# Performance work log

Measured on AMD Instinct MI355X. Metric: run time of the kernel, lower is better.

Reference implementation:

```python
import jax, jax.numpy as jnp
import numpy as np

D_MODEL = 2048
NUM_HEADS = 16
HEAD_DIM = D_MODEL // NUM_HEADS  # 128
B, L = 2, 2048


def setup_inputs() -> dict:
    key = jax.random.key(0)
    ks = jax.random.split(key, 7)
    s = 0.02
    return {
        "x": jax.random.normal(ks[0], (B, L, D_MODEL), dtype=jnp.float32),
        "Wq_w": jax.random.normal(ks[1], (D_MODEL, D_MODEL), dtype=jnp.float32) * s,
        "Wq_b": jnp.zeros((D_MODEL,), dtype=jnp.float32),
        "Wk_w": jax.random.normal(ks[2], (HEAD_DIM, D_MODEL), dtype=jnp.float32) * s,
        "Wk_b": jnp.zeros((HEAD_DIM,), dtype=jnp.float32),
        "Wv_w": jax.random.normal(ks[3], (HEAD_DIM, D_MODEL), dtype=jnp.float32) * s,
        "Wv_b": jnp.zeros((HEAD_DIM,), dtype=jnp.float32),
    }


def reference(x, Wq_w, Wq_b, Wk_w, Wk_b, Wv_w, Wv_b):
    b, l, _ = x.shape
    # torch Linear: y = x @ W.T + b
    Q = (x @ Wq_w.T + Wq_b).reshape(b, l, NUM_HEADS, HEAD_DIM)  # [B,L,H,D]
    K = x @ Wk_w.T + Wk_b  # [B,L,D] single shared KV head (MQA)
    V = x @ Wv_w.T + Wv_b  # [B,L,D]
    scale = 1.0 / jnp.sqrt(jnp.float32(HEAD_DIM))
    # scores: [B,H,Lq,Lk]; K's head dim (size 1 in torch) broadcasts -> contract over d only
    scores = jnp.einsum("bqhd,bkd->bhqk", Q, K) * scale
    attn = jax.nn.softmax(scores, axis=-1)
    out = jnp.einsum("bhqk,bkd->bqhd", attn, V)  # [B,L,H,D]
    return out.reshape(b, l, D_MODEL)
```

## Files before the change

kernel.cpp:

```cpp
#include <hip/hip_runtime.h>
#include <hip/hip_bf16.h>


typedef unsigned short u16;
typedef unsigned int u32;
typedef __bf16 bf16x8 __attribute__((ext_vector_type(8)));
typedef float f32x16 __attribute__((ext_vector_type(16)));
typedef u16 u16x4 __attribute__((ext_vector_type(4)));
typedef u32 u32x4 __attribute__((ext_vector_type(4)));

#define MFMA32(a, b, c) __builtin_amdgcn_mfma_f32_32x32x16_bf16((a), (b), (c), 0, 0, 0)

__device__ __forceinline__ u16 f2bf(float f) {
  __hip_bfloat16 h = __float2bfloat16(f);
  return __builtin_bit_cast(u16, h);
}

__device__ __forceinline__ float fexp2(float x) {
#if __has_builtin(__builtin_amdgcn_exp2f)
  return __builtin_amdgcn_exp2f(x);
#else
  return exp2f(x);
#endif
}

__device__ __forceinline__ void cp16(const void* g, void* l) {
  __builtin_amdgcn_global_load_lds(
      (const __attribute__((address_space(1))) u32*)g,
      (__attribute__((address_space(3))) u32*)l, 16, 0, 0);
}

__device__ __forceinline__ f32x16 zero16() {
  f32x16 v;
#pragma unroll
  for (int i = 0; i < 16; ++i) v[i] = 0.f;
  return v;
}

__global__ __launch_bounds__(256) void k_convert(
    const float* __restrict__ x, const float* __restrict__ wq,
    const float* __restrict__ wk, const float* __restrict__ wv,
    u16* __restrict__ xb, u16* __restrict__ wqb,
    u16* __restrict__ wkb, u16* __restrict__ wvb) {
  int idx = blockIdx.x * 256 + threadIdx.x;
  for (int i = idx; i < 3276800; i += 524288) {
    float4 v; u16* dst;
    if (i < 2097152) {
      v = ((const float4*)x)[i]; dst = xb + (size_t)i * 4;
    } else if (i < 3145728) {
      int j = i - 2097152; v = ((const float4*)wq)[j]; dst = wqb + (size_t)j * 4;
    } else if (i < 3211264) {
      int j = i - 3145728; v = ((const float4*)wk)[j]; dst = wkb + (size_t)j * 4;
    } else {
      int j = i - 3211264; v = ((const float4*)wv)[j]; dst = wvb + (size_t)j * 4;
    }
    u16x4 o;
    o[0] = f2bf(v.x); o[1] = f2bf(v.y); o[2] = f2bf(v.z); o[3] = f2bf(v.w);
    *(u16x4*)dst = o;
  }
}

__global__ __launch_bounds__(256, 2) void k_gemm_qkv(
    const u16* __restrict__ xb, const u16* __restrict__ wqb,
    const u16* __restrict__ wkb, const u16* __restrict__ wvb,
    const float* __restrict__ bq, const float* __restrict__ bk, const float* __restrict__ bv,
    u16* __restrict__ qout, u16* __restrict__ kout, u16* __restrict__ vtout) {
  __shared__ __align__(16) u16 sh[36864];
  const int tid = threadIdx.x;
  const int w = tid >> 6, lane = tid & 63, ln = lane & 31, hi = lane >> 5;
  const int wr = w >> 1, wc = w & 1;
  const int m0 = blockIdx.x * 128;
  const int by = blockIdx.y;
  const int mode = (by < 16) ? 0 : (by - 15);
  const int n0loc = (mode == 0) ? by * 128 : 0;
  const u16* __restrict__ Bp = (mode == 0) ? wqb : (mode == 1 ? wkb : wvb);
  const u16* Arow = xb + (size_t)m0 * 2048;
  const u16* Brow = Bp + (size_t)n0loc * 2048;

  const u16* sb[9];
#pragma unroll
  for (int i = 0; i < 9; ++i) {
    int s = (w + i * 4) * 64 + lane;
    const u16* base; int r, c;
    if (s < 1152) { r = s / 9; c = s % 9; if (c > 7) c = 0; base = Arow; }
    else { int s2 = s - 1152; r = s2 / 9; c = s2 % 9; if (c > 7) c = 0; base = Brow; }
    sb[i] = base + (size_t)r * 2048 + c * 8;
  }

  f32x16 acc[2][2];
  acc[0][0] = zero16(); acc[0][1] = zero16(); acc[1][0] = zero16(); acc[1][1] = zero16();

  const int a0off = (wr * 64 + ln) * 72 + hi * 8;
  const int b0off = 9216 + (wc * 64 + ln) * 72 + hi * 8;

#pragma unroll
  for (int i = 0; i < 9; ++i)
    cp16(sb[i], (void*)(sh + (w + i * 4) * 512));
  __syncthreads();

  for (int it = 0; it < 32; ++it) {
    const int cur = (it & 1) * 18432;
    const int nxt = 18432 - cur;
    const int k0n = (it < 31) ? (it + 1) * 64 : 0;
#pragma unroll
    for (int i = 0; i < 9; ++i)
      cp16(sb[i] + k0n, (void*)(sh + nxt + (w + i * 4) * 512));

#pragma unroll
    for (int kc = 0; kc < 4; ++kc) {
      const int ko = kc * 16;
      bf16x8 a0 = *(const bf16x8*)&sh[cur + a0off + ko];
      bf16x8 a1 = *(const bf16x8*)&sh[cur + a0off + 2304 + ko];
      bf16x8 b0 = *(const bf16x8*)&sh[cur + b0off + ko];
      bf16x8 b1 = *(const bf16x8*)&sh[cur + b0off + 2304 + ko];
      acc[0][0] = MFMA32(a0, b0, acc[0][0]);
      acc[0][1] = MFMA32(a0, b1, acc[0][1]);
      acc[1][0] = MFMA32(a1, b0, acc[1][0]);
      acc[1][1] = MFMA32(a1, b1, acc[1][1]);
    }

    __syncthreads();
  }

  const float qscale = 0.12751744630098356f;
#pragma unroll
  for (int fm = 0; fm < 2; ++fm) {
#pragma unroll
    for (int fn = 0; fn < 2; ++fn) {
      f32x16 a = acc[fm][fn];
      const int mbase = m0 + wr * 64 + fm * 32;
      const int nloc = n0loc + wc * 64 + fn * 32 + ln;
      if (mode == 0) {
        const float bsc = bq[nloc] * qscale;
#pragma unroll
        for (int r = 0; r < 16; ++r) {
          int row = (r & 3) + 8 * (r >> 2) + 4 * hi;
          qout[(size_t)(mbase + row) * 2048 + nloc] = f2bf(a[r] * qscale + bsc);
        }
      } else if (mode == 1) {
        const float bb = bk[nloc];
#pragma unroll
        for (int r = 0; r < 16; ++r) {
          int row = (r & 3) + 8 * (r >> 2) + 4 * hi;
          kout[(size_t)(mbase + row) * 128 + nloc] = f2bf(a[r] + bb);
        }
      } else {
        const float bb = bv[nloc];
#pragma unroll
        for (int r = 0; r < 16; ++r) {
          int row = (r & 3) + 8 * (r >> 2) + 4 * hi;
          int m = mbase + row;
          vtout[(size_t)((m >> 11) * 128 + nloc) * 2048 + (m & 2047)] = f2bf(a[r] + bb);
        }
      }
    }
  }
}

__global__ __launch_bounds__(512, 2) void k_attn(
    const u16* __restrict__ qb, const u16* __restrict__ kb, const u16* __restrict__ vtb,
    float* __restrict__ out) {
  __shared__ __align__(16) u16 sh[35840];
  const int tid = threadIdx.x;
  const int w = tid >> 6, lane = tid & 63, ln = lane & 31, hi = lane >> 5;
  const int q0 = blockIdx.x * 256, h = blockIdx.y, b = blockIdx.z;
  const size_t bL = (size_t)b * 2048;
  const u16* kbase = kb + bL * 128;
  const u16* vbase = vtb + (size_t)b * 128 * 2048;

  bf16x8 qf[8];
  {
    const u16* qrow = qb + (bL + q0 + w * 32 + ln) * 2048 + h * 128 + hi * 8;
#pragma unroll
    for (int kc = 0; kc < 8; ++kc) qf[kc] = *(const bf16x8*)(qrow + kc * 16);
  }

  const u16* sb[5]; int smul[5];
  const int nsl = (w < 3) ? 5 : 4;
#pragma unroll
  for (int i = 0; i < 5; ++i) {
    int sl = w + i * 8;
    if (sl < 35) {
      int s = sl * 64 + lane;
      if (s < 1088) {
        int r = s / 17, c = s % 17; if (c > 15) c = 0;
        sb[i] = kbase + r * 128 + c * 8; smul[i] = 128;
      } else {
        int s2 = s - 1088; int r = s2 / 9, c = s2 % 9; if (c > 7) c = 0;
        sb[i] = vbase + (size_t)r * 2048 + c * 8; smul[i] = 1;
      }
    } else { sb[i] = kbase; smul[i] = 0; }
  }

#pragma unroll
  for (int i = 0; i < 5; ++i)
    if (i < nsl) cp16(sb[i], (void*)(sh + (w + i * 8) * 512));
  __syncthreads();

  f32x16 o[4];
#pragma unroll
  for (int dg = 0; dg < 4; ++dg) o[dg] = zero16();
  float l = 0.f;

  const int kro = ln * 136 + hi * 8;
  const int vro = 8704 + ln * 72 + hi * 8;

  for (int it = 0; it < 32; ++it) {
    const int cur = (it & 1) * 17920;
    const int nxt = 17920 - cur;
    const size_t k0n = (it < 31) ? (size_t)(it + 1) * 64 : 0;
#pragma unroll
    for (int i = 0; i < 5; ++i)
      if (i < nsl) cp16(sb[i] + k0n * smul[i], (void*)(sh + nxt + (w + i * 8) * 512));

    f32x16 s0 = zero16(), s1 = zero16();
#pragma unroll
    for (int kc = 0; kc < 8; ++kc) {
      bf16x8 a0 = *(const bf16x8*)&sh[cur + kro + kc * 16];
      bf16x8 a1 = *(const bf16x8*)&sh[cur + kro + 32 * 136 + kc * 16];
      s0 = MFMA32(a0, qf[kc], s0);
      s1 = MFMA32(a1, qf[kc], s1);
    }

    u32 pk[16];
#pragma unroll
    for (int i = 0; i < 8; ++i) {
      float a = fexp2(s0[2 * i]), c = fexp2(s0[2 * i + 1]);
      pk[i] = __builtin_amdgcn_perm(__builtin_bit_cast(u32, c),
                                    __builtin_bit_cast(u32, a), 0x07060302u);
      float d = fexp2(s1[2 * i]), e = fexp2(s1[2 * i + 1]);
      pk[8 + i] = __builtin_amdgcn_perm(__builtin_bit_cast(u32, e),
                                        __builtin_bit_cast(u32, d), 0x07060302u);
    }
#pragma unroll
    for (int i = 0; i < 16; ++i) {
      l += __builtin_bit_cast(float, pk[i] << 16);
      l += __builtin_bit_cast(float, pk[i] & 0xffff0000u);
    }

    bf16x8 pf[4];
#pragma unroll
    for (int c = 0; c < 4; ++c) {
      const int wb = 4 * c;
      u32 send0 = hi ? pk[wb] : pk[wb + 2];
      u32 send1 = hi ? pk[wb + 1] : pk[wb + 3];
      u32 r0 = (u32)__shfl_xor((int)send0, 32, 64);
      u32 r1 = (u32)__shfl_xor((int)send1, 32, 64);
      u32x4 v;
      v[0] = hi ? r0 : pk[wb];
      v[1] = hi ? r1 : pk[wb + 1];
      v[2] = hi ? pk[wb + 2] : r0;
      v[3] = hi ? pk[wb + 3] : r1;
      pf[c] = __builtin_bit_cast(bf16x8, v);
    }

#pragma unroll
    for (int c = 0; c < 4; ++c)
#pragma unroll
      for (int dg = 0; dg < 4; ++dg) {
        bf16x8 va = *(const bf16x8*)&sh[cur + vro + dg * 2304 + c * 16];
        o[dg] = MFMA32(va, pf[c], o[dg]);
      }

    __syncthreads();
  }

  l += __shfl_xor(l, 32, 64);
  const float inv = 1.0f / l;

  float* orow = out + (bL + q0 + w * 32 + ln) * 2048 + h * 128 + hi * 4;
#pragma unroll
  for (int dg = 0; dg < 4; ++dg)
#pragma unroll
    for (int rq = 0; rq < 4; ++rq) {
      float4 v4;
      v4.x = o[dg][rq * 4 + 0] * inv; v4.y = o[dg][rq * 4 + 1] * inv;
      v4.z = o[dg][rq * 4 + 2] * inv; v4.w = o[dg][rq * 4 + 3] * inv;
      *(float4*)&orow[dg * 32 + rq * 8] = v4;
    }
}

extern "C" void kernel_launch(void* const* d_in, const int* in_sizes, int n_in,
                              void* d_out, int out_size, void* d_ws, size_t ws_size,
                              hipStream_t stream) {
  const float* x  = (const float*)d_in[0];
  const float* wq = (const float*)d_in[1];
  const float* bq = (const float*)d_in[2];
  const float* wk = (const float*)d_in[3];
  const float* bk = (const float*)d_in[4];
  const float* wv = (const float*)d_in[5];
  const float* bv = (const float*)d_in[6];
  float* out = (float*)d_out;
  char* ws = (char*)d_ws;

  u16* xb   = (u16*)(ws);
  u16* wqb  = (u16*)(ws + 16777216);
  u16* wkb  = (u16*)(ws + 25165824);
  u16* wvb  = (u16*)(ws + 25690112);
  u16* qb   = (u16*)(ws + 26214400);
  u16* kbuf = (u16*)(ws + 42991616);
  u16* vtb  = (u16*)(ws + 44040192);

  k_convert<<<2048, 256, 0, stream>>>(x, wq, wk, wv, xb, wqb, wkb, wvb);
  k_gemm_qkv<<<dim3(32, 18), 256, 0, stream>>>(xb, wqb, wkb, wvb, bq, bk, bv, qb, kbuf, vtb);
  k_attn<<<dim3(8, 16, 2), 512, 0, stream>>>(qb, kbuf, vtb, out);
}
```

Measured before the change: 229.5 us.

## Software-pipeline attention loop with triple-buffered LDS and PV lagging one tile

Restructures the attention loop so the P@V MFMAs for the previous tile run while the QK^T and softmax exp for the current tile are computed. A third LDS buffer keeps the previous tile's V alive, raising shared memory from about 70KB to 105KB. It also replaces the perm-based bf16 packing with v_cvt_pk_bf16_f32 (round-to-nearest instead of truncation) and the cross-half shuffles with v_permlane32_swap, and sums the row total l from fp32 values instead of the truncated bf16 ones. The larger LDS footprint may cut blocks per CU below the launch-bounds target of 2.

```diff
diff --git a/kernel.cpp b/kernel.cpp
--- a/kernel.cpp
+++ b/kernel.cpp
@@ -160,7 +160,7 @@
 __global__ __launch_bounds__(512, 2) void k_attn(
     const u16* __restrict__ qb, const u16* __restrict__ kb, const u16* __restrict__ vtb,
     float* __restrict__ out) {
-  __shared__ __align__(16) u16 sh[35840];
+  __shared__ __align__(16) u16 sh[53760];
   const int tid = threadIdx.x;
   const int w = tid >> 6, lane = tid & 63, ln = lane & 31, hi = lane >> 5;
   const int q0 = blockIdx.x * 256, h = blockIdx.y, b = blockIdx.z;
@@ -191,11 +191,13 @@
       }
     } else { sb[i] = kbase; smul[i] = 0; }
   }
+  const int slo = (w)*512;
 
 #pragma unroll
   for (int i = 0; i < 5; ++i)
     if (i < nsl) cp16(sb[i], (void*)(sh + (w + i * 8) * 512));
   __syncthreads();
+  (void)slo;
 
   f32x16 o[4];
 #pragma unroll
@@ -205,65 +207,85 @@
   const int kro = ln * 136 + hi * 8;
   const int vro = 8704 + ln * 72 + hi * 8;
 
-  for (int it = 0; it < 32; ++it) {
-    const int cur = (it & 1) * 17920;
-    const int nxt = 17920 - cur;
-    const size_t k0n = (it < 31) ? (size_t)(it + 1) * 64 : 0;
+  int cA = 0, cN = 17920, cP = 35840;
+  bf16x8 pf[4];
+
+#define SOFTMAX_BODY(PKVAR)                                                   \
+  u32 PKVAR[16];                                                              \
+  _Pragma("unroll") for (int i = 0; i < 8; ++i) {                             \
+    float ea = fexp2(s0[2 * i]), eb = fexp2(s0[2 * i + 1]);                   \
+    float ec = fexp2(s1[2 * i]), ed = fexp2(s1[2 * i + 1]);                   \
+    u32 p0, p1;                                                               \
+    asm("v_cvt_pk_bf16_f32 %0, %1, %2" : "=v"(p0) : "v"(ea), "v"(eb));       \
+    asm("v_cvt_pk_bf16_f32 %0, %1, %2" : "=v"(p1) : "v"(ec), "v"(ed));       \
+    PKVAR[i] = p0; PKVAR[8 + i] = p1;                                         \
+    l += (ea + eb) + (ec + ed);                                               \
+  }                                                                           \
+  _Pragma("unroll") for (int c = 0; c < 4; ++c) {                             \
+    const int wb = 4 * c;                                                     \
+    u32 x0 = PKVAR[wb], y0 = PKVAR[wb + 2];                                   \
+    u32 x1 = PKVAR[wb + 1], y1 = PKVAR[wb + 3];                               \
+    asm("v_permlane32_swap_b32 %0, %1" : "+v"(x0), "+v"(y0));                 \
+    asm("v_permlane32_swap_b32 %0, %1" : "+v"(x1), "+v"(y1));                 \
+    u32x4 vv; vv[0] = x0; vv[1] = x1; vv[2] = y0; vv[3] = y1;                 \
+    pf[c] = __builtin_bit_cast(bf16x8, vv);                                   \
+  }
+
+  {
 #pragma unroll
     for (int i = 0; i < 5; ++i)
-      if (i < nsl) cp16(sb[i] + k0n * smul[i], (void*)(sh + nxt + (w + i * 8) * 512));
+      if (i < nsl) cp16(sb[i] + (size_t)64 * smul[i], (void*)(sh + cN + (w + i * 8) * 512));
 
     f32x16 s0 = zero16(), s1 = zero16();
 #pragma unroll
     for (int kc = 0; kc < 8; ++kc) {
-      bf16x8 a0 = *(const bf16x8*)&sh[cur + kro + kc * 16];
-      bf16x8 a1 = *(const bf16x8*)&sh[cur + kro + 32 * 136 + kc * 16];
+      bf16x8 a0 = *(const bf16x8*)&sh[cA + kro + kc * 16];
+      bf16x8 a1 = *(const bf16x8*)&sh[cA + kro + 32 * 136 + kc * 16];
       s0 = MFMA32(a0, qf[kc], s0);
       s1 = MFMA32(a1, qf[kc], s1);
     }
-
-    u32 pk[16];
-#pragma unroll
-    for (int i = 0; i < 8; ++i) {
-      float a = fexp2(s0[2 * i]), c = fexp2(s0[2 * i + 1]);
-      pk[i] = __builtin_amdgcn_perm(__builtin_bit_cast(u32, c),
-                                    __builtin_bit_cast(u32, a), 0x07060302u);
-      float d = fexp2(s1[2 * i]), e = fexp2(s1[2 * i + 1]);
-      pk[8 + i] = __builtin_amdgcn_perm(__builtin_bit_cast(u32, e),
-                                        __builtin_bit_cast(u32, d), 0x07060302u);
-    }
-#pragma unroll
-    for (int i = 0; i < 16; ++i) {
-      l += __builtin_bit_cast(float, pk[i] << 16);
-      l += __builtin_bit_cast(float, pk[i] & 0xffff0000u);
-    }
-
-    bf16x8 pf[4];
-#pragma unroll
-    for (int c = 0; c < 4; ++c) {
-      const int wb = 4 * c;
-      u32 send0 = hi ? pk[wb] : pk[wb + 2];
-      u32 send1 = hi ? pk[wb + 1] : pk[wb + 3];
-      u32 r0 = (u32)__shfl_xor((int)send0, 32, 64);
-      u32 r1 = (u32)__shfl_xor((int)send1, 32, 64);
-      u32x4 v;
-      v[0] = hi ? r0 : pk[wb];
-      v[1] = hi ? r1 : pk[wb + 1];
-      v[2] = hi ? pk[wb + 2] : r0;
-      v[3] = hi ? pk[wb + 3] : r1;
-      pf[c] = __builtin_bit_cast(bf16x8, v);
+    SOFTMAX_BODY(pk0)
+    __syncthreads();
+    int t = cP; cP = cA; cA = cN; cN = t;
+  }
+
+  for (int it = 1; it < 32; ++it) {
+    const size_t k0n = (it < 31) ? (size_t)(it + 1) * 64 : 0;
+#pragma unroll
+    for (int i = 0; i < 5; ++i)
+      if (i < nsl) cp16(sb[i] + k0n * smul[i], (void*)(sh + cN + (w + i * 8) * 512));
+
+    f32x16 s0 = zero16(), s1 = zero16();
+#pragma unroll
+    for (int kc = 0; kc < 8; ++kc) {
+      bf16x8 a0 = *(const bf16x8*)&sh[cA + kro + kc * 16];
+      bf16x8 a1 = *(const bf16x8*)&sh[cA + kro + 32 * 136 + kc * 16];
+      s0 = MFMA32(a0, qf[kc], s0);
+      s1 = MFMA32(a1, qf[kc], s1);
     }
 
 #pragma unroll
     for (int c = 0; c < 4; ++c)
 #pragma unroll
       for (int dg = 0; dg < 4; ++dg) {
-        bf16x8 va = *(const bf16x8*)&sh[cur + vro + dg * 2304 + c * 16];
+        bf16x8 va = *(const bf16x8*)&sh[cP + vro + dg * 2304 + c * 16];
         o[dg] = MFMA32(va, pf[c], o[dg]);
       }
 
+    SOFTMAX_BODY(pk1)
+
     __syncthreads();
-  }
+    int t = cP; cP = cA; cA = cN; cN = t;
+  }
+
+#pragma unroll
+  for (int c = 0; c < 4; ++c)
+#pragma unroll
+    for (int dg = 0; dg < 4; ++dg) {
+      bf16x8 va = *(const bf16x8*)&sh[cP + vro + dg * 2304 + c * 16];
+      o[dg] = MFMA32(va, pf[c], o[dg]);
+    }
+#undef SOFTMAX_BODY
 
   l += __shfl_xor(l, 32, 64);
   const float inv = 1.0f / l;
```

After: 233.0 us. Within noise of the previous version (+1.5%).

## Split KV tile across wave pairs, each wave covering 64 query rows

Applied to the files above, without the earlier changes.

Each pair of waves now shares 64 query rows and splits every 64-key tile between the two waves, one half each. Each wave reuses each K fragment load for two query sub-tiles and each V fragment for two P fragments. This halves the LDS reads per MFMA in the attention loop. The cost is double the Q and accumulator registers, which pressures occupancy under launch_bounds(512,2), plus an epilogue that reduces partial O and row sums between paired waves through shared memory with extra barriers.

```diff
diff --git a/kernel.cpp b/kernel.cpp
--- a/kernel.cpp
+++ b/kernel.cpp
@@ -163,16 +163,21 @@
   __shared__ __align__(16) u16 sh[35840];
   const int tid = threadIdx.x;
   const int w = tid >> 6, lane = tid & 63, ln = lane & 31, hi = lane >> 5;
+  const int j = w >> 1, kh = w & 1;
   const int q0 = blockIdx.x * 256, h = blockIdx.y, b = blockIdx.z;
   const size_t bL = (size_t)b * 2048;
   const u16* kbase = kb + bL * 128;
   const u16* vbase = vtb + (size_t)b * 128 * 2048;
 
-  bf16x8 qf[8];
+  bf16x8 qfA[8], qfB[8];
   {
-    const u16* qrow = qb + (bL + q0 + w * 32 + ln) * 2048 + h * 128 + hi * 8;
-#pragma unroll
-    for (int kc = 0; kc < 8; ++kc) qf[kc] = *(const bf16x8*)(qrow + kc * 16);
+    const u16* qrowA = qb + (bL + q0 + j * 64 + ln) * 2048 + h * 128 + hi * 8;
+    const u16* qrowB = qrowA + 32 * 2048;
+#pragma unroll
+    for (int kc = 0; kc < 8; ++kc) {
+      qfA[kc] = *(const bf16x8*)(qrowA + kc * 16);
+      qfB[kc] = *(const bf16x8*)(qrowB + kc * 16);
+    }
   }
 
   const u16* sb[5]; int smul[5];
@@ -197,12 +202,12 @@
     if (i < nsl) cp16(sb[i], (void*)(sh + (w + i * 8) * 512));
   __syncthreads();
 
-  f32x16 o[4];
-#pragma unroll
-  for (int dg = 0; dg < 4; ++dg) o[dg] = zero16();
-  float l = 0.f;
-
-  const int kro = ln * 136 + hi * 8;
+  f32x16 oA[4], oB[4];
+#pragma unroll
+  for (int dg = 0; dg < 4; ++dg) { oA[dg] = zero16(); oB[dg] = zero16(); }
+  float lA = 0.f, lB = 0.f;
+
+  const int kro = ln * 136 + hi * 8 + kh * 4352;
   const int vro = 8704 + ln * 72 + hi * 8;
 
   for (int it = 0; it < 32; ++it) {
@@ -213,71 +218,124 @@
     for (int i = 0; i < 5; ++i)
       if (i < nsl) cp16(sb[i] + k0n * smul[i], (void*)(sh + nxt + (w + i * 8) * 512));
 
-    f32x16 s0 = zero16(), s1 = zero16();
+    f32x16 sA = zero16(), sB = zero16();
 #pragma unroll
     for (int kc = 0; kc < 8; ++kc) {
-      bf16x8 a0 = *(const bf16x8*)&sh[cur + kro + kc * 16];
-      bf16x8 a1 = *(const bf16x8*)&sh[cur + kro + 32 * 136 + kc * 16];
-      s0 = MFMA32(a0, qf[kc], s0);
-      s1 = MFMA32(a1, qf[kc], s1);
-    }
-
-    u32 pk[16];
+      bf16x8 a = *(const bf16x8*)&sh[cur + kro + kc * 16];
+      sA = MFMA32(a, qfA[kc], sA);
+      sB = MFMA32(a, qfB[kc], sB);
+    }
+
+    u32 pkA[8], pkB[8];
 #pragma unroll
     for (int i = 0; i < 8; ++i) {
-      float a = fexp2(s0[2 * i]), c = fexp2(s0[2 * i + 1]);
-      pk[i] = __builtin_amdgcn_perm(__builtin_bit_cast(u32, c),
-                                    __builtin_bit_cast(u32, a), 0x07060302u);
-      float d = fexp2(s1[2 * i]), e = fexp2(s1[2 * i + 1]);
-      pk[8 + i] = __builtin_amdgcn_perm(__builtin_bit_cast(u32, e),
-                                        __builtin_bit_cast(u32, d), 0x07060302u);
-    }
-#pragma unroll
-    for (int i = 0; i < 16; ++i) {
-      l += __builtin_bit_cast(float, pk[i] << 16);
-      l += __builtin_bit_cast(float, pk[i] & 0xffff0000u);
-    }
-
-    bf16x8 pf[4];
-#pragma unroll
-    for (int c = 0; c < 4; ++c) {
-      const int wb = 4 * c;
-      u32 send0 = hi ? pk[wb] : pk[wb + 2];
-      u32 send1 = hi ? pk[wb + 1] : pk[wb + 3];
-      u32 r0 = (u32)__shfl_xor((int)send0, 32, 64);
-      u32 r1 = (u32)__shfl_xor((int)send1, 32, 64);
-      u32x4 v;
-      v[0] = hi ? r0 : pk[wb];
-      v[1] = hi ? r1 : pk[wb + 1];
-      v[2] = hi ? pk[wb + 2] : r0;
-      v[3] = hi ? pk[wb + 3] : r1;
-      pf[c] = __builtin_bit_cast(bf16x8, v);
-    }
-
-#pragma unroll
-    for (int c = 0; c < 4; ++c)
+      float a = fexp2(sA[2 * i]), c = fexp2(sA[2 * i + 1]);
+      pkA[i] = __builtin_amdgcn_perm(__builtin_bit_cast(u32, c),
+                                     __builtin_bit_cast(u32, a), 0x07060302u);
+      float d = fexp2(sB[2 * i]), e = fexp2(sB[2 * i + 1]);
+      pkB[i] = __builtin_amdgcn_perm(__builtin_bit_cast(u32, e),
+                                     __builtin_bit_cast(u32, d), 0x07060302u);
+    }
+#pragma unroll
+    for (int i = 0; i < 8; ++i) {
+      lA += __builtin_bit_cast(float, pkA[i] << 16);
+      lA += __builtin_bit_cast(float, pkA[i] & 0xffff0000u);
+      lB += __builtin_bit_cast(float, pkB[i] << 16);
+      lB += __builtin_bit_cast(float, pkB[i] & 0xffff0000u);
+    }
+
+#pragma unroll
+    for (int cp = 0; cp < 2; ++cp) {
+      const int wb = 4 * cp;
+      bf16x8 pfA, pfB;
+      {
+        u32 send0 = hi ? pkA[wb] : pkA[wb + 2];
+        u32 send1 = hi ? pkA[wb + 1] : pkA[wb + 3];
+        u32 r0 = (u32)__shfl_xor((int)send0, 32, 64);
+        u32 r1 = (u32)__shfl_xor((int)send1, 32, 64);
+        u32x4 v;
+        v[0] = hi ? r0 : pkA[wb];
+        v[1] = hi ? r1 : pkA[wb + 1];
+        v[2] = hi ? pkA[wb + 2] : r0;
+        v[3] = hi ? pkA[wb + 3] : r1;
+        pfA = __builtin_bit_cast(bf16x8, v);
+      }
+      {
+        u32 send0 = hi ? pkB[wb] : pkB[wb + 2];
+        u32 send1 = hi ? pkB[wb + 1] : pkB[wb + 3];
+        u32 r0 = (u32)__shfl_xor((int)send0, 32, 64);
+        u32 r1 = (u32)__shfl_xor((int)send1, 32, 64);
+        u32x4 v;
+        v[0] = hi ? r0 : pkB[wb];
+        v[1] = hi ? r1 : pkB[wb + 1];
+        v[2] = hi ? pkB[wb + 2] : r0;
+        v[3] = hi ? pkB[wb + 3] : r1;
+        pfB = __builtin_bit_cast(bf16x8, v);
+      }
+      const int vco = cur + vro + (2 * kh + cp) * 16;
 #pragma unroll
       for (int dg = 0; dg < 4; ++dg) {
-        bf16x8 va = *(const bf16x8*)&sh[cur + vro + dg * 2304 + c * 16];
-        o[dg] = MFMA32(va, pf[c], o[dg]);
-      }
+        bf16x8 va = *(const bf16x8*)&sh[vco + dg * 2304];
+        oA[dg] = MFMA32(va, pfA, oA[dg]);
+        oB[dg] = MFMA32(va, pfB, oB[dg]);
+      }
+    }
 
     __syncthreads();
   }
 
-  l += __shfl_xor(l, 32, 64);
-  const float inv = 1.0f / l;
-
-  float* orow = out + (bL + q0 + w * 32 + ln) * 2048 + h * 128 + hi * 4;
-#pragma unroll
-  for (int dg = 0; dg < 4; ++dg)
-#pragma unroll
-    for (int rq = 0; rq < 4; ++rq) {
-      float4 v4;
-      v4.x = o[dg][rq * 4 + 0] * inv; v4.y = o[dg][rq * 4 + 1] * inv;
-      v4.z = o[dg][rq * 4 + 2] * inv; v4.w = o[dg][rq * 4 + 3] * inv;
-      *(float4*)&orow[dg * 32 + rq * 8] = v4;
-    }
+  lA += __shfl_xor(lA, 32, 64);
+  lB += __shfl_xor(lB, 32, 64);
+  float* lsh = (float*)sh;
+  if (lane < 32) { lsh[w * 64 + ln] = lA; lsh[w * 64 + 32 + ln] = lB; }
+  __syncthreads();
+  float invA = 0.f, invB = 0.f;
+  if (!kh) {
+    invA = 1.0f / (lA + lsh[(w + 1) * 64 + ln]);
+    invB = 1.0f / (lB + lsh[(w + 1) * 64 + 32 + ln]);
+  }
+  __syncthreads();
+  float* po0 = (float*)(sh + 1024);
+#pragma unroll
+  for (int ph = 0; ph < 2; ++ph) {
+    if (kh == 1 && (j >> 1) == ph) {
+      float* po = po0 + (j & 1) * 8192;
+#pragma unroll
+      for (int g = 0; g < 16; ++g) {
+        float4 va, vb;
+        va.x = oA[g >> 2][(g & 3) * 4 + 0]; va.y = oA[g >> 2][(g & 3) * 4 + 1];
+        va.z = oA[g >> 2][(g & 3) * 4 + 2]; va.w = oA[g >> 2][(g & 3) * 4 + 3];
+        vb.x = oB[g >> 2][(g & 3) * 4 + 0]; vb.y = oB[g >> 2][(g & 3) * 4 + 1];
+        vb.z = oB[g >> 2][(g & 3) * 4 + 2]; vb.w = oB[g >> 2][(g & 3) * 4 + 3];
+        *(float4*)&po[(g * 64 + lane) * 4] = va;
+        *(float4*)&po[((16 + g) * 64 + lane) * 4] = vb;
+      }
+    }
+    __syncthreads();
+    if (kh == 0 && (j >> 1) == ph) {
+      float* po = po0 + (j & 1) * 8192;
+      float* orowA = out + (bL + q0 + j * 64 + ln) * 2048 + h * 128 + hi * 4;
+      float* orowB = orowA + 32 * 2048;
+#pragma unroll
+      for (int g = 0; g < 16; ++g) {
+        const int dg = g >> 2, rq = g & 3;
+        float4 pa = *(const float4*)&po[(g * 64 + lane) * 4];
+        float4 pb = *(const float4*)&po[((16 + g) * 64 + lane) * 4];
+        float4 va, vb;
+        va.x = (oA[dg][rq * 4 + 0] + pa.x) * invA;
+        va.y = (oA[dg][rq * 4 + 1] + pa.y) * invA;
+        va.z = (oA[dg][rq * 4 + 2] + pa.z) * invA;
+        va.w = (oA[dg][rq * 4 + 3] + pa.w) * invA;
+        vb.x = (oB[dg][rq * 4 + 0] + pb.x) * invB;
+        vb.y = (oB[dg][rq * 4 + 1] + pb.y) * invB;
+        vb.z = (oB[dg][rq * 4 + 2] + pb.z) * invB;
+        vb.w = (oB[dg][rq * 4 + 3] + pb.w) * invB;
+        *(float4*)&orowA[dg * 32 + rq * 8] = va;
+        *(float4*)&orowB[dg * 32 + rq * 8] = vb;
+      }
+    }
+    __syncthreads();
+  }
 }
 
 extern "C" void kernel_launch(void* const* d_in, const int* in_sizes, int n_in,
```

Result: slower. 236.2 us (+2.9%).

## Use 256x256 tiles for Q projection GEMM with separate K/V tile path

Applied to the files above, without the earlier changes.

The Q projection GEMM now uses 256x256 output tiles per block (4x4 MFMA fragments per wave) with doubled shared memory, while K and V projections keep 128-row tiles, launched as a flat 1D grid of 192 blocks. Larger tiles raise arithmetic intensity and cut redundant global/LDS loads of x and Wq. In exchange occupancy drops to one block per CU, register pressure rises with 256 accumulator floats per lane, and only 128 Q blocks exist for 256 CUs, which can leave many CUs idle.

```diff
diff --git a/kernel.cpp b/kernel.cpp
--- a/kernel.cpp
+++ b/kernel.cpp
@@ -60,22 +60,102 @@
   }
 }
 
-__global__ __launch_bounds__(256, 2) void k_gemm_qkv(
+__global__ __launch_bounds__(256, 1) void k_gemm_qkv(
     const u16* __restrict__ xb, const u16* __restrict__ wqb,
     const u16* __restrict__ wkb, const u16* __restrict__ wvb,
     const float* __restrict__ bq, const float* __restrict__ bk, const float* __restrict__ bv,
     u16* __restrict__ qout, u16* __restrict__ kout, u16* __restrict__ vtout) {
-  __shared__ __align__(16) u16 sh[36864];
+  __shared__ __align__(16) u16 sh[73728];
   const int tid = threadIdx.x;
   const int w = tid >> 6, lane = tid & 63, ln = lane & 31, hi = lane >> 5;
   const int wr = w >> 1, wc = w & 1;
-  const int m0 = blockIdx.x * 128;
-  const int by = blockIdx.y;
-  const int mode = (by < 16) ? 0 : (by - 15);
-  const int n0loc = (mode == 0) ? by * 128 : 0;
-  const u16* __restrict__ Bp = (mode == 0) ? wqb : (mode == 1 ? wkb : wvb);
+  const int id = blockIdx.x;
+  const float qscale = 0.12751744630098356f;
+
+  if (id < 128) {
+    const int m0 = (id >> 3) * 256, n0 = (id & 7) * 256;
+    const u16* Arow = xb + (size_t)m0 * 2048;
+    const u16* Brow = wqb + (size_t)n0 * 2048;
+
+    const u16* sb[18];
+#pragma unroll
+    for (int i = 0; i < 18; ++i) {
+      int s = (w + i * 4) * 64 + lane;
+      const u16* base; int r, c;
+      if (s < 2304) { r = s / 9; c = s % 9; if (c > 7) c = 0; base = Arow; }
+      else { int s2 = s - 2304; r = s2 / 9; c = s2 % 9; if (c > 7) c = 0; base = Brow; }
+      sb[i] = base + (size_t)r * 2048 + c * 8;
+    }
+
+    f32x16 acc[4][4];
+#pragma unroll
+    for (int am = 0; am < 4; ++am)
+#pragma unroll
+      for (int an = 0; an < 4; ++an) acc[am][an] = zero16();
+
+    int aoff[4], boff[4];
+#pragma unroll
+    for (int t = 0; t < 4; ++t) {
+      aoff[t] = (wr * 128 + t * 32 + ln) * 72 + hi * 8;
+      boff[t] = 18432 + (wc * 128 + t * 32 + ln) * 72 + hi * 8;
+    }
+
+#pragma unroll
+    for (int i = 0; i < 18; ++i)
+      cp16(sb[i], (void*)(sh + (w + i * 4) * 512));
+    __syncthreads();
+
+    for (int it = 0; it < 32; ++it) {
+      const int cur = (it & 1) * 36864;
+      const int nxt = 36864 - cur;
+      const int k0n = (it < 31) ? (it + 1) * 64 : 0;
+#pragma unroll
+      for (int i = 0; i < 18; ++i)
+        cp16(sb[i] + k0n, (void*)(sh + nxt + (w + i * 4) * 512));
+
+#pragma unroll
+      for (int kc = 0; kc < 4; ++kc) {
+        const int ko = kc * 16;
+        bf16x8 af[4], bfr[4];
+#pragma unroll
+        for (int t = 0; t < 4; ++t) {
+          af[t]  = *(const bf16x8*)&sh[cur + aoff[t] + ko];
+          bfr[t] = *(const bf16x8*)&sh[cur + boff[t] + ko];
+        }
+#pragma unroll
+        for (int am = 0; am < 4; ++am)
+#pragma unroll
+          for (int an = 0; an < 4; ++an)
+            acc[am][an] = MFMA32(af[am], bfr[an], acc[am][an]);
+      }
+
+      __syncthreads();
+    }
+
+#pragma unroll
+    for (int am = 0; am < 4; ++am) {
+      const int mbase = m0 + wr * 128 + am * 32;
+#pragma unroll
+      for (int an = 0; an < 4; ++an) {
+        const int nloc = n0 + wc * 128 + an * 32 + ln;
+        const float bsc = bq[nloc] * qscale;
+        f32x16 a = acc[am][an];
+#pragma unroll
+        for (int r = 0; r < 16; ++r) {
+          int row = (r & 3) + 8 * (r >> 2) + 4 * hi;
+          qout[(size_t)(mbase + row) * 2048 + nloc] = f2bf(a[r] * qscale + bsc);
+        }
+      }
+    }
+    return;
+  }
+
+  const int id2 = id - 128;
+  const int mode = 1 + (id2 >> 5);
+  const int m0 = (id2 & 31) * 128;
+  const u16* __restrict__ Bp = (mode == 1) ? wkb : wvb;
   const u16* Arow = xb + (size_t)m0 * 2048;
-  const u16* Brow = Bp + (size_t)n0loc * 2048;
+  const u16* Brow = Bp;
 
   const u16* sb[9];
 #pragma unroll
@@ -122,22 +202,14 @@
     __syncthreads();
   }
 
-  const float qscale = 0.12751744630098356f;
 #pragma unroll
   for (int fm = 0; fm < 2; ++fm) {
 #pragma unroll
     for (int fn = 0; fn < 2; ++fn) {
       f32x16 a = acc[fm][fn];
       const int mbase = m0 + wr * 64 + fm * 32;
-      const int nloc = n0loc + wc * 64 + fn * 32 + ln;
-      if (mode == 0) {
-        const float bsc = bq[nloc] * qscale;
-#pragma unroll
-        for (int r = 0; r < 16; ++r) {
-          int row = (r & 3) + 8 * (r >> 2) + 4 * hi;
-          qout[(size_t)(mbase + row) * 2048 + nloc] = f2bf(a[r] * qscale + bsc);
-        }
-      } else if (mode == 1) {
+      const int nloc = wc * 64 + fn * 32 + ln;
+      if (mode == 1) {
         const float bb = bk[nloc];
 #pragma unroll
         for (int r = 0; r < 16; ++r) {
@@ -302,6 +374,6 @@
   u16* vtb  = (u16*)(ws + 44040192);
 
   k_convert<<<2048, 256, 0, stream>>>(x, wq, wk, wv, xb, wqb, wkb, wvb);
-  k_gemm_qkv<<<dim3(32, 18), 256, 0, stream>>>(xb, wqb, wkb, wvb, bq, bk, bv, qb, kbuf, vtb);
+  k_gemm_qkv<<<192, 256, 0, stream>>>(xb, wqb, wkb, wvb, bq, bk, bv, qb, kbuf, vtb);
   k_attn<<<dim3(8, 16, 2), 512, 0, stream>>>(qb, kbuf, vtb, out);
 }
```

New measurement: 241.2 us. 1.05x slower.
